# Kernel optimization log

Measured on AMD Instinct MI355X. Metric: run time of the kernel, lower is better.

## Reference

```python
import jax, jax.numpy as jnp
import numpy as np

DT = 1.0          # integration timestep (ms)
SIGMA = 0.5       # gauss_std for surrogate (unused in pure fwd spike)
AMPLITUDE = 0.3   # dampening_factor
N = 50000         # neurons
R = 4             # receptor types
D = 5             # max_delay
E = 5000000       # recurrent synapses
B = 4             # batch


def setup_inputs() -> dict:
    key = jax.random.key(0)
    ks = jax.random.split(key, 20)
    f = jnp.float32
    inputs = jax.random.normal(ks[0], (B, N * R), f) * 0.1
    # z_buf holds binary spikes for the last D steps
    z_buf = jax.random.bernoulli(ks[1], 0.05, (B, N * D)).astype(f)
    v = jax.random.uniform(ks[2], (B, N), f, 0.0, 1.0)
    r = jnp.zeros((B, N), f)
    asc_1 = jax.random.normal(ks[3], (B, N), f)
    asc_2 = jax.random.normal(ks[4], (B, N), f)
    psc_rise = jax.random.normal(ks[5], (B, N * R), f) * 0.5
    psc = jax.random.normal(ks[6], (B, N * R), f)
    rec_w = jax.random.normal(ks[7], (E,), f) * 0.01
    rec_rows = jax.random.randint(ks[8], (E,), 0, N * R, jnp.int32)
    rec_cols = jax.random.randint(ks[9], (E,), 0, N * D, jnp.int32)
    syn_decay = jax.random.uniform(ks[10], (N, R), f, 0.5, 0.99)
    psc_initial = jax.random.uniform(ks[11], (N, R), f, 0.1, 1.0)
    t_ref = jax.random.uniform(ks[12], (N,), f, 1.0, 4.0)
    asc_amps = jax.random.normal(ks[13], (N, 2), f)
    k = jax.random.normal(ks[14], (N, 2), f)  # inv-sigmoid space, read via sigmoid
    v_th = jnp.ones((N,), f)
    e_l = jnp.zeros((N,), f)
    v_reset = jnp.zeros((N,), f)
    g = jax.random.uniform(ks[15], (N,), f, 0.1, 1.0)
    decay = jax.random.uniform(ks[16], (N,), f, 0.8, 0.99)
    current_factor = jax.random.uniform(ks[17], (N,), f, 0.1, 1.0)
    voltage_scale = jnp.ones((N,), f) * 20.0
    voltage_offset = jnp.ones((N,), f) * -70.0
    return dict(inputs=inputs, z_buf=z_buf, v=v, r=r, asc_1=asc_1, asc_2=asc_2,
                psc_rise=psc_rise, psc=psc, rec_w=rec_w, rec_rows=rec_rows,
                rec_cols=rec_cols, syn_decay=syn_decay, psc_initial=psc_initial,
                t_ref=t_ref, asc_amps=asc_amps, k=k, v_th=v_th, e_l=e_l,
                v_reset=v_reset, g=g, decay=decay, current_factor=current_factor,
                voltage_scale=voltage_scale, voltage_offset=voltage_offset)


def _step(inputs, z_buf, v, r, asc_1, asc_2, psc_rise, psc,
          rec_w, rec_rows, rec_cols, syn_decay, psc_initial, t_ref,
          asc_amps, k, v_th, e_l, v_reset, g, decay, current_factor,
          voltage_scale, voltage_offset):
    shaped_z_buf = z_buf.reshape(B, D, N)
    prev_z = shaped_z_buf[:, 0]                      # most recent spikes [B,N]
    psc_rise_r = psc_rise.reshape(B, N, R)
    psc_r = psc.reshape(B, N, R)

    # sparse recurrent matmul: W[N*R, N*D] @ z_buf^T -> [N*R, B]
    vals = rec_w[:, None] * z_buf.T[rec_cols]        # [E, B] gather
    i_rec = jax.ops.segment_sum(vals, rec_rows, num_segments=N * R).T  # [B, N*R]

    rec_inputs = (i_rec + inputs).reshape(B, N, R)
    new_psc_rise = syn_decay * psc_rise_r + rec_inputs * psc_initial
    new_psc = psc_r * syn_decay + DT * syn_decay * psc_rise_r

    new_r = jax.nn.relu(r + prev_z * t_ref - DT)

    kk = jax.nn.sigmoid(k)                           # param_k_read()
    new_asc_1 = jnp.exp(-DT * kk[:, 0]) * asc_1 + prev_z * asc_amps[:, 0]
    new_asc_2 = jnp.exp(-DT * kk[:, 1]) * asc_2 + prev_z * asc_amps[:, 1]

    reset_current = prev_z * (v_reset - v_th)
    input_current = psc_r.sum(-1)                    # old psc
    c1 = input_current + asc_1 + asc_2 + g * e_l
    new_v = decay * v + current_factor * c1 + reset_current

    v_sc = (new_v - v_th) / (v_th - e_l)
    new_z = (v_sc > 0.0).astype(v_sc.dtype)          # spike_gauss forward
    new_z = jnp.where(new_r > 0.0, jnp.zeros_like(new_z), new_z)

    new_z_buf = jnp.concatenate([new_z[:, None], shaped_z_buf[:, :-1]], axis=1)
    out_v = new_v * voltage_scale + voltage_offset
    return (new_z, out_v, new_r, new_asc_1, new_asc_2,
            new_psc_rise.reshape(B, N * R), new_psc.reshape(B, N * R),
            new_z_buf.reshape(B, N * D))


def reference(inputs, z_buf, v, r, asc_1, asc_2, psc_rise, psc,
              rec_w, rec_rows, rec_cols, syn_decay, psc_initial, t_ref,
              asc_amps, k, v_th, e_l, v_reset, g, decay, current_factor,
              voltage_scale, voltage_offset):
    outs = _step(inputs, z_buf, v, r, asc_1, asc_2, psc_rise, psc,
                 rec_w, rec_rows, rec_cols, syn_decay, psc_initial, t_ref,
                 asc_amps, k, v_th, e_l, v_reset, g, decay, current_factor,
                 voltage_scale, voltage_offset)
    # pack outputs + new state into one [B, N*(5+2R+D)] array
    return jnp.concatenate(outs, axis=-1)
```

## Files before the change

kernel.cpp:

```cpp
#include <hip/hip_runtime.h>

#define Nn 50000
#define Rr 4
#define Dd 5
#define Ee 5000000
#define Bb 4
#define NRr (Nn * Rr)
#define NDd (Nn * Dd)
#define ZW 7814
#define OUT_STRIDE (18 * Nn)

struct P {
    const float* inputs; const float* z_buf; const float* v; const float* r;
    const float* asc1; const float* asc2; const float* psc_rise; const float* psc;
    const float* rec_w; const int* rec_rows; const int* rec_cols;
    const float* syn_decay; const float* psc_initial; const float* t_ref;
    const float* asc_amps; const float* k; const float* v_th; const float* e_l;
    const float* v_reset; const float* g; const float* decay;
    const float* current_factor; const float* vscale; const float* voffset;
    float* out; unsigned char* z_pack; unsigned* zbits;
};

__global__ __launch_bounds__(256) void pack_neuron_kernel(P p) {
    int i = blockIdx.x * 256 + threadIdx.x;

    unsigned m = 0;
    if (i < NDd) {
#pragma unroll
        for (int b = 0; b < Bb; ++b)
            if (p.z_buf[(size_t)b * NDd + i] != 0.0f) m |= (1u << b);
        p.z_pack[i] = (unsigned char)m;
    }
    unsigned long long bal = __ballot(m != 0);
    if ((i & 63) == 0 && i < NDd) {
        p.zbits[(i >> 5)]     = (unsigned)bal;
        p.zbits[(i >> 5) + 1] = (unsigned)(bal >> 32);
    }

    if (i < Bb * Nn) {
        int b = i / Nn;
        int n = i - b * Nn;
        const size_t bn  = (size_t)b * Nn + n;
        const size_t bnr = (size_t)b * NRr + (size_t)n * 4;

        float prev_z = p.z_buf[(size_t)b * NDd + n];
        float4 pr  = *(const float4*)(p.psc_rise + bnr);
        float4 pc  = *(const float4*)(p.psc + bnr);
        float4 in4 = *(const float4*)(p.inputs + bnr);
        float4 sd  = *(const float4*)(p.syn_decay + (size_t)n * 4);
        float4 pi  = *(const float4*)(p.psc_initial + (size_t)n * 4);

        float4 nprb;
        nprb.x = sd.x * pr.x + in4.x * pi.x;
        nprb.y = sd.y * pr.y + in4.y * pi.y;
        nprb.z = sd.z * pr.z + in4.z * pi.z;
        nprb.w = sd.w * pr.w + in4.w * pi.w;

        float4 npc;
        npc.x = pc.x * sd.x + sd.x * pr.x;
        npc.y = pc.y * sd.y + sd.y * pr.y;
        npc.z = pc.z * sd.z + sd.z * pr.z;
        npc.w = pc.w * sd.w + sd.w * pr.w;
        float input_current = pc.x + pc.y + pc.z + pc.w;

        float new_r = fmaxf(p.r[bn] + prev_z * p.t_ref[n] - 1.0f, 0.0f);

        float2 kv = *(const float2*)(p.k + (size_t)n * 2);
        float2 aa = *(const float2*)(p.asc_amps + (size_t)n * 2);
        float kk0 = 1.0f / (1.0f + expf(-kv.x));
        float kk1 = 1.0f / (1.0f + expf(-kv.y));
        float a1 = p.asc1[bn];
        float a2 = p.asc2[bn];
        float na1 = expf(-kk0) * a1 + prev_z * aa.x;
        float na2 = expf(-kk1) * a2 + prev_z * aa.y;

        float vth = p.v_th[n];
        float el  = p.e_l[n];
        float reset_current = prev_z * (p.v_reset[n] - vth);
        float c1 = input_current + a1 + a2 + p.g[n] * el;
        float new_v = p.decay[n] * p.v[bn] + p.current_factor[n] * c1
                      + reset_current;
        float v_sc = (new_v - vth) / (vth - el);
        float new_z = (v_sc > 0.0f) ? 1.0f : 0.0f;
        if (new_r > 0.0f) new_z = 0.0f;
        float out_v = new_v * p.vscale[n] + p.voffset[n];

        float* ob = p.out + (size_t)b * OUT_STRIDE;
        ob[n]          = new_z;
        ob[Nn + n]     = out_v;
        ob[2 * Nn + n] = new_r;
        ob[3 * Nn + n] = na1;
        ob[4 * Nn + n] = na2;
        *(float4*)(ob + 5 * Nn + (size_t)n * 4) = nprb;
        *(float4*)(ob + 9 * Nn + (size_t)n * 4) = npc;
        ob[13 * Nn + n] = new_z;
#pragma unroll
        for (int d = 0; d < Dd - 1; ++d)
            ob[14 * Nn + (size_t)d * Nn + n] =
                p.z_buf[(size_t)b * NDd + (size_t)d * Nn + n];
    }
}

__global__ __launch_bounds__(256) void edge_kernel(P p) {
    __shared__ unsigned zb[ZW];
    for (int t = threadIdx.x; t < ZW; t += 256) zb[t] = p.zbits[t];
    __syncthreads();
    const int tid = blockIdx.x * 256 + threadIdx.x;
    if (tid >= Ee / 4) return;

    int4 c = ((const int4*)p.rec_cols)[tid];
    unsigned h0 = (zb[(unsigned)c.x >> 5] >> (c.x & 31)) & 1u;
    unsigned h1 = (zb[(unsigned)c.y >> 5] >> (c.y & 31)) & 1u;
    unsigned h2 = (zb[(unsigned)c.z >> 5] >> (c.z & 31)) & 1u;
    unsigned h3 = (zb[(unsigned)c.w >> 5] >> (c.w & 31)) & 1u;
    if (!(h0 | h1 | h2 | h3)) return;

    int4 rw = ((const int4*)p.rec_rows)[tid];
    float4 w = ((const float4*)p.rec_w)[tid];
    float* o5 = p.out + 5 * Nn;
    auto do_edge = [&](unsigned hh, int col, int row, float wv) {
        if (hh) {
            unsigned mm = p.z_pack[col];
            if (mm) {
                float wp = wv * p.psc_initial[row];
                if (mm & 1u) atomicAdd(o5 + 0 * OUT_STRIDE + row, wp);
                if (mm & 2u) atomicAdd(o5 + 1 * OUT_STRIDE + row, wp);
                if (mm & 4u) atomicAdd(o5 + 2 * OUT_STRIDE + row, wp);
                if (mm & 8u) atomicAdd(o5 + 3 * OUT_STRIDE + row, wp);
            }
        }
    };
    do_edge(h0, c.x, rw.x, w.x);
    do_edge(h1, c.y, rw.y, w.y);
    do_edge(h2, c.z, rw.z, w.z);
    do_edge(h3, c.w, rw.w, w.w);
}

extern "C" void kernel_launch(void* const* d_in, const int* in_sizes, int n_in,
                              void* d_out, int out_size, void* d_ws, size_t ws_size,
                              hipStream_t stream) {
    P p;
    p.inputs        = (const float*)d_in[0];
    p.z_buf         = (const float*)d_in[1];
    p.v             = (const float*)d_in[2];
    p.r             = (const float*)d_in[3];
    p.asc1          = (const float*)d_in[4];
    p.asc2          = (const float*)d_in[5];
    p.psc_rise      = (const float*)d_in[6];
    p.psc           = (const float*)d_in[7];
    p.rec_w         = (const float*)d_in[8];
    p.rec_rows      = (const int*)d_in[9];
    p.rec_cols      = (const int*)d_in[10];
    p.syn_decay     = (const float*)d_in[11];
    p.psc_initial   = (const float*)d_in[12];
    p.t_ref         = (const float*)d_in[13];
    p.asc_amps      = (const float*)d_in[14];
    p.k             = (const float*)d_in[15];
    p.v_th          = (const float*)d_in[16];
    p.e_l           = (const float*)d_in[17];
    p.v_reset       = (const float*)d_in[18];
    p.g             = (const float*)d_in[19];
    p.decay         = (const float*)d_in[20];
    p.current_factor= (const float*)d_in[21];
    p.vscale        = (const float*)d_in[22];
    p.voffset       = (const float*)d_in[23];
    p.out           = (float*)d_out;
    p.z_pack = (unsigned char*)d_ws;
    p.zbits  = (unsigned*)((char*)d_ws + ((NDd + 255) & ~255));

    pack_neuron_kernel<<<(NDd + 255) / 256, 256, 0, stream>>>(p);
    edge_kernel<<<(Ee / 4 + 255) / 256, 256, 0, stream>>>(p);
}
```

Measured before the change: 204.7 us.

## Privatize scatter accumulators per XCC and reduce in a separate kernel

Edge-kernel atomics now target one of eight per-XCC private copies of the psc_rise accumulator, selected by reading the hardware XCC id. This lets them use workgroup-scope atomics and avoids cross-die coherence traffic to a single output array. The psc_initial multiply is moved out of the per-edge path into a new reduction kernel, which sums the copies and computes psc_rise. The cost is zeroing 8×3.2MB of workspace, an extra kernel launch and an extra reduction pass. Correctness relies on workgroup-scope atomics staying coherent within an XCC's shared L2.

After: 212.6 us. 3.8% more time.

```diff
diff --git a/kernel.cpp b/kernel.cpp
--- a/kernel.cpp
+++ b/kernel.cpp
@@ -9,6 +9,7 @@
 #define NDd (Nn * Dd)
 #define ZW 7814
 #define OUT_STRIDE (18 * Nn)
+#define CSTR (Bb * NRr)
 
 struct P {
     const float* inputs; const float* z_buf; const float* v; const float* r;
@@ -18,11 +19,17 @@
     const float* asc_amps; const float* k; const float* v_th; const float* e_l;
     const float* v_reset; const float* g; const float* decay;
     const float* current_factor; const float* vscale; const float* voffset;
-    float* out; unsigned char* z_pack; unsigned* zbits;
+    float* out; float* copies; unsigned char* z_pack; unsigned* zbits;
+    int ncopies;
 };
 
 __global__ __launch_bounds__(256) void pack_neuron_kernel(P p) {
     int i = blockIdx.x * 256 + threadIdx.x;
+    int nthreads = gridDim.x * 256;
+
+    int nz4 = p.ncopies * CSTR / 4;
+    for (int t = i; t < nz4; t += nthreads)
+        ((float4*)p.copies)[t] = make_float4(0.f, 0.f, 0.f, 0.f);
 
     unsigned m = 0;
     if (i < NDd) {
@@ -44,17 +51,9 @@
         const size_t bnr = (size_t)b * NRr + (size_t)n * 4;
 
         float prev_z = p.z_buf[(size_t)b * NDd + n];
-        float4 pr  = *(const float4*)(p.psc_rise + bnr);
-        float4 pc  = *(const float4*)(p.psc + bnr);
-        float4 in4 = *(const float4*)(p.inputs + bnr);
-        float4 sd  = *(const float4*)(p.syn_decay + (size_t)n * 4);
-        float4 pi  = *(const float4*)(p.psc_initial + (size_t)n * 4);
-
-        float4 nprb;
-        nprb.x = sd.x * pr.x + in4.x * pi.x;
-        nprb.y = sd.y * pr.y + in4.y * pi.y;
-        nprb.z = sd.z * pr.z + in4.z * pi.z;
-        nprb.w = sd.w * pr.w + in4.w * pi.w;
+        float4 pr = *(const float4*)(p.psc_rise + bnr);
+        float4 pc = *(const float4*)(p.psc + bnr);
+        float4 sd = *(const float4*)(p.syn_decay + (size_t)n * 4);
 
         float4 npc;
         npc.x = pc.x * sd.x + sd.x * pr.x;
@@ -91,7 +90,6 @@
         ob[2 * Nn + n] = new_r;
         ob[3 * Nn + n] = na1;
         ob[4 * Nn + n] = na2;
-        *(float4*)(ob + 5 * Nn + (size_t)n * 4) = nprb;
         *(float4*)(ob + 9 * Nn + (size_t)n * 4) = npc;
         ob[13 * Nn + n] = new_z;
 #pragma unroll
@@ -108,6 +106,16 @@
     const int tid = blockIdx.x * 256 + threadIdx.x;
     if (tid >= Ee / 4) return;
 
+    float* my;
+    bool priv = (p.ncopies == 8);
+    if (priv) {
+        unsigned xcc;
+        asm volatile("s_getreg_b32 %0, hwreg(HW_REG_XCC_ID)" : "=s"(xcc));
+        my = p.copies + (size_t)(xcc & 7u) * CSTR;
+    } else {
+        my = p.copies;
+    }
+
     int4 c = ((const int4*)p.rec_cols)[tid];
     unsigned h0 = (zb[(unsigned)c.x >> 5] >> (c.x & 31)) & 1u;
     unsigned h1 = (zb[(unsigned)c.y >> 5] >> (c.y & 31)) & 1u;
@@ -117,23 +125,52 @@
 
     int4 rw = ((const int4*)p.rec_rows)[tid];
     float4 w = ((const float4*)p.rec_w)[tid];
-    float* o5 = p.out + 5 * Nn;
+
+    auto acc = [&](int idx, float wv) {
+        if (priv)
+            __hip_atomic_fetch_add(&my[idx], wv, __ATOMIC_RELAXED,
+                                   __HIP_MEMORY_SCOPE_WORKGROUP);
+        else
+            atomicAdd(&my[idx], wv);
+    };
     auto do_edge = [&](unsigned hh, int col, int row, float wv) {
         if (hh) {
             unsigned mm = p.z_pack[col];
-            if (mm) {
-                float wp = wv * p.psc_initial[row];
-                if (mm & 1u) atomicAdd(o5 + 0 * OUT_STRIDE + row, wp);
-                if (mm & 2u) atomicAdd(o5 + 1 * OUT_STRIDE + row, wp);
-                if (mm & 4u) atomicAdd(o5 + 2 * OUT_STRIDE + row, wp);
-                if (mm & 8u) atomicAdd(o5 + 3 * OUT_STRIDE + row, wp);
-            }
+            if (mm & 1u) acc(0 * NRr + row, wv);
+            if (mm & 2u) acc(1 * NRr + row, wv);
+            if (mm & 4u) acc(2 * NRr + row, wv);
+            if (mm & 8u) acc(3 * NRr + row, wv);
         }
     };
     do_edge(h0, c.x, rw.x, w.x);
     do_edge(h1, c.y, rw.y, w.y);
     do_edge(h2, c.z, rw.z, w.z);
     do_edge(h3, c.w, rw.w, w.w);
+}
+
+__global__ __launch_bounds__(256) void psc_rise_kernel(P p) {
+    int tid = blockIdx.x * 256 + threadIdx.x;
+    if (tid >= Bb * Nn) return;
+    int b = tid / Nn;
+    int n = tid - b * Nn;
+    const size_t bnr = (size_t)b * NRr + (size_t)n * 4;
+
+    float4 s = make_float4(0.f, 0.f, 0.f, 0.f);
+    for (int c = 0; c < p.ncopies; ++c) {
+        float4 t = *(const float4*)(p.copies + (size_t)c * CSTR + bnr);
+        s.x += t.x; s.y += t.y; s.z += t.z; s.w += t.w;
+    }
+    float4 in4 = *(const float4*)(p.inputs + bnr);
+    float4 pr  = *(const float4*)(p.psc_rise + bnr);
+    float4 sd  = *(const float4*)(p.syn_decay + (size_t)n * 4);
+    float4 pi  = *(const float4*)(p.psc_initial + (size_t)n * 4);
+    float4 npr;
+    npr.x = sd.x * pr.x + (s.x + in4.x) * pi.x;
+    npr.y = sd.y * pr.y + (s.y + in4.y) * pi.y;
+    npr.z = sd.z * pr.z + (s.z + in4.z) * pi.z;
+    npr.w = sd.w * pr.w + (s.w + in4.w) * pi.w;
+    float* ob = p.out + (size_t)b * OUT_STRIDE;
+    *(float4*)(ob + 5 * Nn + (size_t)n * 4) = npr;
 }
 
 extern "C" void kernel_launch(void* const* d_in, const int* in_sizes, int n_in,
@@ -165,9 +202,14 @@
     p.vscale        = (const float*)d_in[22];
     p.voffset       = (const float*)d_in[23];
     p.out           = (float*)d_out;
-    p.z_pack = (unsigned char*)d_ws;
-    p.zbits  = (unsigned*)((char*)d_ws + ((NDd + 255) & ~255));
+
+    const size_t need8 = (size_t)8 * CSTR * 4 + 250112 + 4 * ZW;
+    p.ncopies = (ws_size >= need8) ? 8 : 1;
+    p.copies  = (float*)d_ws;
+    p.z_pack  = (unsigned char*)d_ws + (size_t)p.ncopies * CSTR * 4;
+    p.zbits   = (unsigned*)((char*)p.z_pack + 250112);
 
     pack_neuron_kernel<<<(NDd + 255) / 256, 256, 0, stream>>>(p);
     edge_kernel<<<(Ee / 4 + 255) / 256, 256, 0, stream>>>(p);
-}
+    psc_rise_kernel<<<(Bb * Nn + 255) / 256, 256, 0, stream>>>(p);
+}
```
